# Optimization experiments

Hardware: AMD Instinct MI355X
Metric: run time of the kernel (lower is better)

Reference implementation:

```python
import jax, jax.numpy as jnp
import numpy as np

ALPHA = 4.0  # spikingjelly surrogate.Sigmoid default alpha

@jax.custom_vjp
def heaviside_sg(x):
    # forward: Heaviside (spike); backward: sigmoid surrogate gradient
    return (x >= 0.0).astype(x.dtype)

def _h_fwd(x):
    return heaviside_sg(x), x

def _h_bwd(x, g):
    s = jax.nn.sigmoid(ALPHA * x)
    return (g * ALPHA * s * (1.0 - s),)

heaviside_sg.defvjp(_h_fwd, _h_bwd)

def lif_wta_step(v, x, tau, vth):
    # charge (decay_input=False, v_reset=0): v = v + x - v/tau
    v = v + x - v / tau
    # winner-take-all fire: only the per-sample argmax neuron may spike
    mask = jax.nn.one_hot(jnp.argmax(v, axis=1), v.shape[1], dtype=v.dtype)
    spike = heaviside_sg(v * mask - vth)
    pre_v = v  # membrane before reset (stored as pre_v)
    # overridden neuronal_reset: reset spike computed WITHOUT WTA mask; hard reset to 0
    reset_spike = heaviside_sg(v - vth)
    v_next = v * (1.0 - reset_spike)
    return v_next, spike, pre_v

def setup_inputs() -> dict:
    key = jax.random.key(0)
    k1, k2, k3 = jax.random.split(key, 3)
    B, C, T = 256, 32, 4000
    x = jax.random.normal(k1, (B, C, T), dtype=jnp.float32)
    # init: normal(mean=0.8, std=0.05) then clamp to [0,1]
    W1 = jnp.clip(0.8 + 0.05 * jax.random.normal(k2, (64, 32), dtype=jnp.float32), 0.0, 1.0)
    W2 = jnp.clip(0.8 + 0.05 * jax.random.normal(k3, (128, 64), dtype=jnp.float32), 0.0, 1.0)
    return {"x": x, "W1": W1, "W2": W2}

def reference(x, W1, W2):
    B = x.shape[0]
    dt = x.dtype
    xt = jnp.transpose(x, (2, 0, 1))  # [T, B, 32]
    carry0 = (jnp.zeros((B, 32), dt), jnp.zeros((B, 64), dt),
              jnp.zeros((B, 128), dt), jnp.zeros((B, 128), dt))

    def step(carry, inp):
        v0, v1, v2, _ = carry
        v0n, s0, _ = lif_wta_step(v0, inp, 3.0, 1.5)      # trans_neuron
        h1 = s0 @ W1.T                                    # [B,64]
        v1n, s1, _ = lif_wta_step(v1, h1, 80000.0, 1.2)   # b1_neuron
        h2 = s1 @ W2.T                                    # [B,128]
        v2n, _, pv2 = lif_wta_step(v2, h2, 80000.0, 1.2)  # b2_neuron
        return (v0n, v1n, v2n, pv2), None

    (_, _, _, pre_v2), _ = jax.lax.scan(step, carry0, xt)
    return jnp.exp(pre_v2)  # liquid_state: exp of last-step pre-reset membrane of b2
```

## Files before the change

### kernel.cpp

```cpp
#include <hip/hip_runtime.h>
#include <cstdint>
#include <cstddef>


#pragma clang fp contract(off)

typedef float f32x4 __attribute__((ext_vector_type(4)));

constexpr int T_TOTAL = 4000;
constexpr int NCH = 32;
constexpr int N1 = 64;
constexpr int N2 = 128;
constexpr int CT = 96;
constexpr int TS0 = 108;
constexpr int TS1 = 100;
constexpr int NCHUNK = (T_TOTAL + CT - 1) / CT;

__device__ __forceinline__ int read_lane_i(int v, int l) {
  return __builtin_amdgcn_readlane(v, l);
}

__global__ __launch_bounds__(512, 1) void lsm_kernel(
    const float* __restrict__ x, const float* __restrict__ W1,
    const float* __restrict__ W2, float* __restrict__ out) {
  __shared__ float w1s[N1 * 33];
  __shared__ float w2s[N2 * 65];
  __shared__ float xs[2][NCH * TS0];
  __shared__ float nv0r[2][NCH * TS1];
  __shared__ float nv1r[2][N1 * TS1];
  __shared__ unsigned j0r[2][CT];
  __shared__ float mpr[2][2][CT];
  __shared__ int   jpr[2][2][CT];

  const int tid = threadIdx.x;
  const int wid = tid >> 6;
  const int lane = tid & 63;
  const int b = blockIdx.x;

  for (int e = tid; e < N1 * NCH; e += 512) w1s[(e >> 5) * 33 + (e & 31)] = W1[e];
  for (int e = tid; e < N2 * N1; e += 512) w2s[(e >> 6) * 65 + (e & 63)] = W2[e];
  if (tid < N1) w1s[tid * 33 + 32] = 0.f;
  if (tid < N2) w2s[tid * 65 + 64] = 0.f;
  __syncthreads();

  const float* xb = x + (size_t)b * (NCH * T_TOTAL);
  constexpr float R3 = 1.0f / 3.0f;
  constexpr float R80 = 1.0f / 80000.0f;

  float nv0p = 0.f;
  float nv1p = 0.f;
  float nv2p = 0.f;

  for (int p = 0; p < NCHUNK + 5; ++p) {
    if (wid == 0) {
      const int c = p - 1;
      if (c >= 0 && c < NCHUNK) {
        const int S = min(CT, T_TOTAL - c * CT);
        const int xl = lane & 31;
        const int hi4 = (lane >> 5) << 2;
        const float* xrow = xs[c & 1] + xl * TS0;
        float* nrow = nv0r[c & 1] + xl * TS1 + hi4;
        f32x4 C0 = *(const f32x4*)(xrow + 0);
        f32x4 C1 = *(const f32x4*)(xrow + 4);
        for (int tb = 0; tb < S; tb += 8) {
          f32x4 N0 = *(const f32x4*)(xrow + tb + 8);
          f32x4 Nx = *(const f32x4*)(xrow + tb + 12);
          float nva[8];
#pragma unroll
          for (int k = 0; k < 8; ++k) {
            float xc = (k < 4) ? C0[k] : C1[k - 4];
            float a  = nv0p + xc;
            float q0 = nv0p * R3;
            float e  = __builtin_fmaf(-3.0f, q0, nv0p);
            float q  = __builtin_fmaf(e, R3, q0);
            bool  r  = nv0p >= 1.5f;
            float f  = a - q;
            nv0p = r ? xc : f;
            nva[k] = nv0p;
          }
          f32x4 wv;
          wv.x = hi4 ? nva[4] : nva[0];
          wv.y = hi4 ? nva[5] : nva[1];
          wv.z = hi4 ? nva[6] : nva[2];
          wv.w = hi4 ? nva[7] : nva[3];
          *(f32x4*)(nrow + tb) = wv;
          C0 = N0; C1 = Nx;
        }
      }
    } else if (wid == 1) {
      const int c = p - 2;
      if (c >= 0 && c < NCHUNK) {
        const int cb = c & 1;
        const float* nvs = nv0r[cb] + lane;
        float m = nvs[0];
        int j = 0;
#pragma unroll 8
        for (int n = 1; n < 32; ++n) {
          float v = nvs[n * TS1];
          bool g = v > m;
          j = g ? n : j;
          m = g ? v : m;
        }
        j0r[cb][lane] = (m >= 1.5f) ? (unsigned)j : 32u;
        if (lane < 32) {
          const float* nvs2 = nv0r[cb] + 64 + lane;
          float m2 = nvs2[0];
          int j2 = 0;
#pragma unroll 8
          for (int n = 1; n < 32; ++n) {
            float v = nvs2[n * TS1];
            bool g = v > m2;
            j2 = g ? n : j2;
            m2 = g ? v : m2;
          }
          j0r[cb][64 + lane] = (m2 >= 1.5f) ? (unsigned)j2 : 32u;
        }
      }
    } else if (wid == 2) {
      const int c = p - 3;
      if (c >= 0 && c < NCHUNK) {
        const int S = min(CT, T_TOTAL - c * CT);
        const int cb = c & 1;
        const int jv  = (int)j0r[cb][lane];
        const int jv2 = (int)j0r[cb][64 + (lane & 31)];
        const float* wrow = w1s + lane * 33;
        float* nrow = nv1r[cb] + lane * TS1;
        float hr[8];
#pragma unroll
        for (int k = 0; k < 8; ++k) hr[k] = wrow[read_lane_i(jv, k)];
        for (int tb = 0; tb < S; tb += 8) {
          const int pb = tb + 8;
          const bool hi = pb >= 64;
          const int src = hi ? jv2 : jv;
          const int pbase = hi ? pb - 64 : pb;
          float nva[8];
#pragma unroll
          for (int k = 0; k < 8; ++k) {
            float h = hr[k];
            hr[k] = wrow[read_lane_i(src, pbase + k)];
            float a = nv1p + h;
            float m = nv1p * R80;
            bool  r = nv1p >= 1.2f;
            float f = a - m;
            nv1p = r ? h : f;
            nva[k] = nv1p;
          }
          f32x4 w0v = {nva[0], nva[1], nva[2], nva[3]};
          f32x4 w1v = {nva[4], nva[5], nva[6], nva[7]};
          *(f32x4*)(nrow + tb) = w0v;
          *(f32x4*)(nrow + tb + 4) = w1v;
        }
      }
    } else if (wid == 3 || wid == 6) {
      const int c = p - 4;
      if (c >= 0 && c < NCHUNK) {
        const int cb = c & 1;
        const int half = (wid == 6) ? 1 : 0;
        const float* nvs = nv1r[cb] + half * 32 * TS1 + lane;
        float m = nvs[0];
        int j = 0;
#pragma unroll 8
        for (int n = 1; n < 32; ++n) {
          float v = nvs[n * TS1];
          bool g = v > m;
          j = g ? n : j;
          m = g ? v : m;
        }
        mpr[cb][half][lane] = m;
        jpr[cb][half][lane] = j;
        if (lane < 32) {
          const float* nvs2 = nv1r[cb] + half * 32 * TS1 + 64 + lane;
          float m2 = nvs2[0];
          int j2 = 0;
#pragma unroll 8
          for (int n = 1; n < 32; ++n) {
            float v = nvs2[n * TS1];
            bool g = v > m2;
            j2 = g ? n : j2;
            m2 = g ? v : m2;
          }
          mpr[cb][half][64 + lane] = m2;
          jpr[cb][half][64 + lane] = j2;
        }
      }
    } else if (wid == 4) {
      const int c = p;
      if (c < NCHUNK) {
        float* dst = xs[c & 1];
        const int g8 = lane >> 3;
        const int tl8 = (lane & 7) << 2;
        f32x4 vr[12];
        bool okv[12];
#pragma unroll
        for (int j = 0; j < 12; ++j) {
          const int k = (j & 3) * 8 + g8;
          const int ts = j >> 2;
          const int tg = c * CT + ts * 32 + tl8;
          const bool ok = (tg + 3) < T_TOTAL;
          okv[j] = ok;
          const int tgs = ok ? tg : 0;
          vr[j] = *reinterpret_cast<const f32x4*>(&xb[(size_t)k * T_TOTAL + tgs]);
        }
#pragma unroll
        for (int j = 0; j < 12; ++j) {
          if (okv[j]) {
            const int k = (j & 3) * 8 + g8;
            const int ts = j >> 2;
            *(f32x4*)(&dst[k * TS0 + ts * 32 + tl8]) = vr[j];
          }
        }
      }
    } else {
      const int c = p - 5;
      if (c >= 0 && c < NCHUNK) {
        const int S = min(CT, T_TOTAL - c * CT);
        const int cb = c & 1;
        float mlo = mpr[cb][0][lane], mhi = mpr[cb][1][lane];
        int jlo = jpr[cb][0][lane], jhi = jpr[cb][1][lane];
        bool g = mhi > mlo;
        float mm = g ? mhi : mlo;
        int jj = g ? (jhi + 32) : jlo;
        const int pkv = (mm >= 1.2f) ? jj : 64;
        const int l32 = 64 + (lane & 31);
        float mlo2 = mpr[cb][0][l32], mhi2 = mpr[cb][1][l32];
        int jlo2 = jpr[cb][0][l32], jhi2 = jpr[cb][1][l32];
        bool g2 = mhi2 > mlo2;
        float mm2 = g2 ? mhi2 : mlo2;
        int jj2 = g2 ? (jhi2 + 32) : jlo2;
        const int pkv2 = (mm2 >= 1.2f) ? jj2 : 64;
        const float* wrow = w2s + (lane + ((wid == 7) ? 64 : 0)) * 65;
        float hr[8];
#pragma unroll
        for (int k = 0; k < 8; ++k) hr[k] = wrow[read_lane_i(pkv, k)];
        for (int tb = 0; tb < S; tb += 8) {
          const int pb = tb + 8;
          const bool hi = pb >= 64;
          const int src = hi ? pkv2 : pkv;
          const int pbase = hi ? pb - 64 : pb;
#pragma unroll
          for (int k = 0; k < 8; ++k) {
            float h = hr[k];
            hr[k] = wrow[read_lane_i(src, pbase + k)];
            float a = nv2p + h;
            float m = nv2p * R80;
            bool  r = nv2p >= 1.2f;
            float f = a - m;
            nv2p = r ? h : f;
          }
        }
      }
    }
    __syncthreads();
  }

  if (wid == 5) out[(size_t)b * N2 + lane] = expf(nv2p);
  if (wid == 7) out[(size_t)b * N2 + 64 + lane] = expf(nv2p);
}

extern "C" void kernel_launch(void* const* d_in, const int* in_sizes, int n_in,
                              void* d_out, int out_size, void* d_ws, size_t ws_size,
                              hipStream_t stream) {
  (void)n_in; (void)out_size; (void)d_ws; (void)ws_size;
  const float* x = (const float*)d_in[0];
  const float* W1 = (const float*)d_in[1];
  const float* W2 = (const float*)d_in[2];
  float* out = (float*)d_out;
  const int B = in_sizes[0] / (NCH * T_TOTAL);
  lsm_kernel<<<dim3(B), dim3(512), 0, stream>>>(x, W1, W2, out);
}
```

Before: 277.7 us.

## Shorten wavefront pipeline: direct global x loads, fused argmax stages, L2 prefetch

Removes the shared-memory x staging stage: warp 0 now reads x directly from global memory with a two-deep register prefetch. The layer-0 argmax is fused into the layer-1 warp, and each argmax warp now handles all 128 timesteps. These changes cut the pipeline from NCHUNK+5 to NCHUNK+3 barrier phases. Chunk size grows from 96 to 128 timesteps to amortize barriers, and warps 1 and 4 become touch-loaders that warm the cache for the next chunk. The risk is global-load latency on warp 0's serial recurrence and longer per-phase critical paths.

```diff
diff --git a/kernel.cpp b/kernel.cpp
--- a/kernel.cpp
+++ b/kernel.cpp
@@ -11,9 +11,8 @@
 constexpr int NCH = 32;
 constexpr int N1 = 64;
 constexpr int N2 = 128;
-constexpr int CT = 96;
-constexpr int TS0 = 108;
-constexpr int TS1 = 100;
+constexpr int CT = 128;
+constexpr int TS1 = 140;
 constexpr int NCHUNK = (T_TOTAL + CT - 1) / CT;
 
 __device__ __forceinline__ int read_lane_i(int v, int l) {
@@ -25,10 +24,8 @@
     const float* __restrict__ W2, float* __restrict__ out) {
   __shared__ float w1s[N1 * 33];
   __shared__ float w2s[N2 * 65];
-  __shared__ float xs[2][NCH * TS0];
   __shared__ float nv0r[2][NCH * TS1];
   __shared__ float nv1r[2][N1 * TS1];
-  __shared__ unsigned j0r[2][CT];
   __shared__ float mpr[2][2][CT];
   __shared__ int   jpr[2][2][CT];
 
@@ -50,21 +47,26 @@
   float nv0p = 0.f;
   float nv1p = 0.f;
   float nv2p = 0.f;
-
-  for (int p = 0; p < NCHUNK + 5; ++p) {
+  float warm = 0.f;
+
+  for (int p = 0; p < NCHUNK + 3; ++p) {
     if (wid == 0) {
-      const int c = p - 1;
-      if (c >= 0 && c < NCHUNK) {
+      const int c = p;
+      if (c < NCHUNK) {
         const int S = min(CT, T_TOTAL - c * CT);
         const int xl = lane & 31;
         const int hi4 = (lane >> 5) << 2;
-        const float* xrow = xs[c & 1] + xl * TS0;
+        const float* xg = xb + (size_t)xl * T_TOTAL + c * CT;
         float* nrow = nv0r[c & 1] + xl * TS1 + hi4;
-        f32x4 C0 = *(const f32x4*)(xrow + 0);
-        f32x4 C1 = *(const f32x4*)(xrow + 4);
+        const int tmax = T_TOTAL - c * CT - 8;
+        f32x4 C0 = *(const f32x4*)(xg + 0);
+        f32x4 C1 = *(const f32x4*)(xg + 4);
+        f32x4 D0 = *(const f32x4*)(xg + 8);
+        f32x4 D1 = *(const f32x4*)(xg + 12);
         for (int tb = 0; tb < S; tb += 8) {
-          f32x4 N0 = *(const f32x4*)(xrow + tb + 8);
-          f32x4 Nx = *(const f32x4*)(xrow + tb + 12);
+          int tp = tb + 16; tp = (tp < tmax) ? tp : tmax;
+          f32x4 E0 = *(const f32x4*)(xg + tp);
+          f32x4 E1 = *(const f32x4*)(xg + tp + 4);
           float nva[8];
 #pragma unroll
           for (int k = 0; k < 8; ++k) {
@@ -84,12 +86,13 @@
           wv.z = hi4 ? nva[6] : nva[2];
           wv.w = hi4 ? nva[7] : nva[3];
           *(f32x4*)(nrow + tb) = wv;
-          C0 = N0; C1 = Nx;
-        }
-      }
-    } else if (wid == 1) {
-      const int c = p - 2;
+          C0 = D0; C1 = D1; D0 = E0; D1 = E1;
+        }
+      }
+    } else if (wid == 2) {
+      const int c = p - 1;
       if (c >= 0 && c < NCHUNK) {
+        const int S = min(CT, T_TOTAL - c * CT);
         const int cb = c & 1;
         const float* nvs = nv0r[cb] + lane;
         float m = nvs[0];
@@ -101,28 +104,18 @@
           j = g ? n : j;
           m = g ? v : m;
         }
-        j0r[cb][lane] = (m >= 1.5f) ? (unsigned)j : 32u;
-        if (lane < 32) {
-          const float* nvs2 = nv0r[cb] + 64 + lane;
-          float m2 = nvs2[0];
-          int j2 = 0;
-#pragma unroll 8
-          for (int n = 1; n < 32; ++n) {
-            float v = nvs2[n * TS1];
-            bool g = v > m2;
-            j2 = g ? n : j2;
-            m2 = g ? v : m2;
-          }
-          j0r[cb][64 + lane] = (m2 >= 1.5f) ? (unsigned)j2 : 32u;
-        }
-      }
-    } else if (wid == 2) {
-      const int c = p - 3;
-      if (c >= 0 && c < NCHUNK) {
-        const int S = min(CT, T_TOTAL - c * CT);
-        const int cb = c & 1;
-        const int jv  = (int)j0r[cb][lane];
-        const int jv2 = (int)j0r[cb][64 + (lane & 31)];
+        const int jv = (m >= 1.5f) ? j : 32;
+        const float* nvs2 = nv0r[cb] + 64 + lane;
+        float m2 = nvs2[0];
+        int j2 = 0;
+#pragma unroll 8
+        for (int n = 1; n < 32; ++n) {
+          float v = nvs2[n * TS1];
+          bool g = v > m2;
+          j2 = g ? n : j2;
+          m2 = g ? v : m2;
+        }
+        const int jv2 = (m2 >= 1.5f) ? j2 : 32;
         const float* wrow = w1s + lane * 33;
         float* nrow = nv1r[cb] + lane * TS1;
         float hr[8];
@@ -139,9 +132,9 @@
             float h = hr[k];
             hr[k] = wrow[read_lane_i(src, pbase + k)];
             float a = nv1p + h;
-            float m = nv1p * R80;
+            float mm = nv1p * R80;
             bool  r = nv1p >= 1.2f;
-            float f = a - m;
+            float f = a - mm;
             nv1p = r ? h : f;
             nva[k] = nv1p;
           }
@@ -152,7 +145,7 @@
         }
       }
     } else if (wid == 3 || wid == 6) {
-      const int c = p - 4;
+      const int c = p - 2;
       if (c >= 0 && c < NCHUNK) {
         const int cb = c & 1;
         const int half = (wid == 6) ? 1 : 0;
@@ -168,50 +161,30 @@
         }
         mpr[cb][half][lane] = m;
         jpr[cb][half][lane] = j;
-        if (lane < 32) {
-          const float* nvs2 = nv1r[cb] + half * 32 * TS1 + 64 + lane;
-          float m2 = nvs2[0];
-          int j2 = 0;
-#pragma unroll 8
-          for (int n = 1; n < 32; ++n) {
-            float v = nvs2[n * TS1];
-            bool g = v > m2;
-            j2 = g ? n : j2;
-            m2 = g ? v : m2;
-          }
-          mpr[cb][half][64 + lane] = m2;
-          jpr[cb][half][64 + lane] = j2;
-        }
-      }
-    } else if (wid == 4) {
-      const int c = p;
-      if (c < NCHUNK) {
-        float* dst = xs[c & 1];
-        const int g8 = lane >> 3;
-        const int tl8 = (lane & 7) << 2;
-        f32x4 vr[12];
-        bool okv[12];
-#pragma unroll
-        for (int j = 0; j < 12; ++j) {
-          const int k = (j & 3) * 8 + g8;
-          const int ts = j >> 2;
-          const int tg = c * CT + ts * 32 + tl8;
-          const bool ok = (tg + 3) < T_TOTAL;
-          okv[j] = ok;
-          const int tgs = ok ? tg : 0;
-          vr[j] = *reinterpret_cast<const f32x4*>(&xb[(size_t)k * T_TOTAL + tgs]);
-        }
-#pragma unroll
-        for (int j = 0; j < 12; ++j) {
-          if (okv[j]) {
-            const int k = (j & 3) * 8 + g8;
-            const int ts = j >> 2;
-            *(f32x4*)(&dst[k * TS0 + ts * 32 + tl8]) = vr[j];
-          }
-        }
+        const float* nvs2 = nvs + 64;
+        float m2 = nvs2[0];
+        int j2 = 0;
+#pragma unroll 8
+        for (int n = 1; n < 32; ++n) {
+          float v = nvs2[n * TS1];
+          bool g = v > m2;
+          j2 = g ? n : j2;
+          m2 = g ? v : m2;
+        }
+        mpr[cb][half][64 + lane] = m2;
+        jpr[cb][half][64 + lane] = j2;
+      }
+    } else if (wid == 1 || wid == 4) {
+      const int c2 = p + 1;
+      if (c2 < NCHUNK) {
+        const int L = lane + ((wid == 4) ? 64 : 0);
+        const int ch = L >> 2;
+        int t = c2 * CT + (L & 3) * 32;
+        t = (t < T_TOTAL) ? t : (T_TOTAL - 1);
+        warm += xb[(size_t)ch * T_TOTAL + t];
       }
     } else {
-      const int c = p - 5;
+      const int c = p - 3;
       if (c >= 0 && c < NCHUNK) {
         const int S = min(CT, T_TOTAL - c * CT);
         const int cb = c & 1;
@@ -221,9 +194,8 @@
         float mm = g ? mhi : mlo;
         int jj = g ? (jhi + 32) : jlo;
         const int pkv = (mm >= 1.2f) ? jj : 64;
-        const int l32 = 64 + (lane & 31);
-        float mlo2 = mpr[cb][0][l32], mhi2 = mpr[cb][1][l32];
-        int jlo2 = jpr[cb][0][l32], jhi2 = jpr[cb][1][l32];
+        float mlo2 = mpr[cb][0][64 + lane], mhi2 = mpr[cb][1][64 + lane];
+        int jlo2 = jpr[cb][0][64 + lane], jhi2 = jpr[cb][1][64 + lane];
         bool g2 = mhi2 > mlo2;
         float mm2 = g2 ? mhi2 : mlo2;
         int jj2 = g2 ? (jhi2 + 32) : jlo2;
@@ -242,9 +214,9 @@
             float h = hr[k];
             hr[k] = wrow[read_lane_i(src, pbase + k)];
             float a = nv2p + h;
-            float m = nv2p * R80;
+            float mv = nv2p * R80;
             bool  r = nv2p >= 1.2f;
-            float f = a - m;
+            float f = a - mv;
             nv2p = r ? h : f;
           }
         }
@@ -255,6 +227,7 @@
 
   if (wid == 5) out[(size_t)b * N2 + lane] = expf(nv2p);
   if (wid == 7) out[(size_t)b * N2 + 64 + lane] = expf(nv2p);
+  asm volatile("" :: "v"(warm));
 }
 
 extern "C" void kernel_launch(void* const* d_in, const int* in_sizes, int n_in,
```

New measurement: 326.0 us. 1.17x slower.

## Replace block-wide barriers with per-stage LDS flag producer/consumer synchronization

Applied to the files above, without the earlier changes.

Replaces the lockstep pipeline, where every chunk ends with __syncthreads across all eight waves, with point-to-point producer/consumer flags in volatile shared memory. Each wave now spins (with s_sleep) only on the stages it depends on and on its double-buffer consumers, so stages no longer wait on the slowest wave every chunk. The layer-0 argmax is also folded into the layer-1 wave, which removes the j0r buffer and the separate wave-1 stage. This adds spin-wait and LDS polling overhead, and it relies on correct memory ordering through the waitcnt and volatile flags.

```diff
diff --git a/kernel.cpp b/kernel.cpp
--- a/kernel.cpp
+++ b/kernel.cpp
@@ -16,6 +16,9 @@
 constexpr int TS1 = 100;
 constexpr int NCHUNK = (T_TOTAL + CT - 1) / CT;
 
+constexpr int P1 = 0, C1 = 1, P2 = 2, C2 = 3, P4 = 4, C4A = 5, C4B = 6,
+              P5 = 7, C5A = 8, C5B = 9, P6 = 10, C6A = 11, C6B = 12;
+
 __device__ __forceinline__ int read_lane_i(int v, int l) {
   return __builtin_amdgcn_readlane(v, l);
 }
@@ -28,9 +31,9 @@
   __shared__ float xs[2][NCH * TS0];
   __shared__ float nv0r[2][NCH * TS1];
   __shared__ float nv1r[2][N1 * TS1];
-  __shared__ unsigned j0r[2][CT];
   __shared__ float mpr[2][2][CT];
   __shared__ int   jpr[2][2][CT];
+  volatile __shared__ int fl[16];
 
   const int tid = threadIdx.x;
   const int wid = tid >> 6;
@@ -41,220 +44,243 @@
   for (int e = tid; e < N2 * N1; e += 512) w2s[(e >> 6) * 65 + (e & 63)] = W2[e];
   if (tid < N1) w1s[tid * 33 + 32] = 0.f;
   if (tid < N2) w2s[tid * 65 + 64] = 0.f;
+  if (tid < 16) fl[tid] = 0;
   __syncthreads();
+
+  auto wait_ge = [&](int idx, int tgt) {
+    if (tgt <= 0) return;
+    while (fl[idx] < tgt) __builtin_amdgcn_s_sleep(1);
+    asm volatile("" ::: "memory");
+    __builtin_amdgcn_sched_barrier(0);
+  };
+  auto publish = [&](int idx, int val) {
+    __builtin_amdgcn_sched_barrier(0);
+    asm volatile("s_waitcnt lgkmcnt(0)" ::: "memory");
+    if (lane == 0) fl[idx] = val;
+  };
 
   const float* xb = x + (size_t)b * (NCH * T_TOTAL);
   constexpr float R3 = 1.0f / 3.0f;
   constexpr float R80 = 1.0f / 80000.0f;
 
-  float nv0p = 0.f;
-  float nv1p = 0.f;
-  float nv2p = 0.f;
-
-  for (int p = 0; p < NCHUNK + 5; ++p) {
-    if (wid == 0) {
-      const int c = p - 1;
-      if (c >= 0 && c < NCHUNK) {
-        const int S = min(CT, T_TOTAL - c * CT);
-        const int xl = lane & 31;
-        const int hi4 = (lane >> 5) << 2;
-        const float* xrow = xs[c & 1] + xl * TS0;
-        float* nrow = nv0r[c & 1] + xl * TS1 + hi4;
-        f32x4 C0 = *(const f32x4*)(xrow + 0);
-        f32x4 C1 = *(const f32x4*)(xrow + 4);
-        for (int tb = 0; tb < S; tb += 8) {
-          f32x4 N0 = *(const f32x4*)(xrow + tb + 8);
-          f32x4 Nx = *(const f32x4*)(xrow + tb + 12);
-          float nva[8];
-#pragma unroll
-          for (int k = 0; k < 8; ++k) {
-            float xc = (k < 4) ? C0[k] : C1[k - 4];
-            float a  = nv0p + xc;
-            float q0 = nv0p * R3;
-            float e  = __builtin_fmaf(-3.0f, q0, nv0p);
-            float q  = __builtin_fmaf(e, R3, q0);
-            bool  r  = nv0p >= 1.5f;
-            float f  = a - q;
-            nv0p = r ? xc : f;
-            nva[k] = nv0p;
-          }
-          f32x4 wv;
-          wv.x = hi4 ? nva[4] : nva[0];
-          wv.y = hi4 ? nva[5] : nva[1];
-          wv.z = hi4 ? nva[6] : nva[2];
-          wv.w = hi4 ? nva[7] : nva[3];
-          *(f32x4*)(nrow + tb) = wv;
-          C0 = N0; C1 = Nx;
-        }
-      }
-    } else if (wid == 1) {
-      const int c = p - 2;
-      if (c >= 0 && c < NCHUNK) {
-        const int cb = c & 1;
-        const float* nvs = nv0r[cb] + lane;
-        float m = nvs[0];
-        int j = 0;
-#pragma unroll 8
-        for (int n = 1; n < 32; ++n) {
-          float v = nvs[n * TS1];
-          bool g = v > m;
-          j = g ? n : j;
-          m = g ? v : m;
-        }
-        j0r[cb][lane] = (m >= 1.5f) ? (unsigned)j : 32u;
-        if (lane < 32) {
-          const float* nvs2 = nv0r[cb] + 64 + lane;
-          float m2 = nvs2[0];
-          int j2 = 0;
-#pragma unroll 8
-          for (int n = 1; n < 32; ++n) {
-            float v = nvs2[n * TS1];
-            bool g = v > m2;
-            j2 = g ? n : j2;
-            m2 = g ? v : m2;
-          }
-          j0r[cb][64 + lane] = (m2 >= 1.5f) ? (unsigned)j2 : 32u;
-        }
-      }
-    } else if (wid == 2) {
-      const int c = p - 3;
-      if (c >= 0 && c < NCHUNK) {
-        const int S = min(CT, T_TOTAL - c * CT);
-        const int cb = c & 1;
-        const int jv  = (int)j0r[cb][lane];
-        const int jv2 = (int)j0r[cb][64 + (lane & 31)];
-        const float* wrow = w1s + lane * 33;
-        float* nrow = nv1r[cb] + lane * TS1;
-        float hr[8];
-#pragma unroll
-        for (int k = 0; k < 8; ++k) hr[k] = wrow[read_lane_i(jv, k)];
-        for (int tb = 0; tb < S; tb += 8) {
-          const int pb = tb + 8;
-          const bool hi = pb >= 64;
-          const int src = hi ? jv2 : jv;
-          const int pbase = hi ? pb - 64 : pb;
-          float nva[8];
-#pragma unroll
-          for (int k = 0; k < 8; ++k) {
-            float h = hr[k];
-            hr[k] = wrow[read_lane_i(src, pbase + k)];
-            float a = nv1p + h;
-            float m = nv1p * R80;
-            bool  r = nv1p >= 1.2f;
-            float f = a - m;
-            nv1p = r ? h : f;
-            nva[k] = nv1p;
-          }
-          f32x4 w0v = {nva[0], nva[1], nva[2], nva[3]};
-          f32x4 w1v = {nva[4], nva[5], nva[6], nva[7]};
-          *(f32x4*)(nrow + tb) = w0v;
-          *(f32x4*)(nrow + tb + 4) = w1v;
-        }
-      }
-    } else if (wid == 3 || wid == 6) {
-      const int c = p - 4;
-      if (c >= 0 && c < NCHUNK) {
-        const int cb = c & 1;
-        const int half = (wid == 6) ? 1 : 0;
-        const float* nvs = nv1r[cb] + half * 32 * TS1 + lane;
-        float m = nvs[0];
-        int j = 0;
-#pragma unroll 8
-        for (int n = 1; n < 32; ++n) {
-          float v = nvs[n * TS1];
-          bool g = v > m;
-          j = g ? n : j;
-          m = g ? v : m;
-        }
-        mpr[cb][half][lane] = m;
-        jpr[cb][half][lane] = j;
-        if (lane < 32) {
-          const float* nvs2 = nv1r[cb] + half * 32 * TS1 + 64 + lane;
-          float m2 = nvs2[0];
-          int j2 = 0;
-#pragma unroll 8
-          for (int n = 1; n < 32; ++n) {
-            float v = nvs2[n * TS1];
-            bool g = v > m2;
-            j2 = g ? n : j2;
-            m2 = g ? v : m2;
-          }
-          mpr[cb][half][64 + lane] = m2;
-          jpr[cb][half][64 + lane] = j2;
-        }
-      }
-    } else if (wid == 4) {
-      const int c = p;
-      if (c < NCHUNK) {
-        float* dst = xs[c & 1];
-        const int g8 = lane >> 3;
-        const int tl8 = (lane & 7) << 2;
-        f32x4 vr[12];
-        bool okv[12];
-#pragma unroll
-        for (int j = 0; j < 12; ++j) {
+  if (wid == 4) {
+    const int g8 = lane >> 3;
+    const int tl8 = (lane & 7) << 2;
+    for (int c = 0; c < NCHUNK; ++c) {
+      wait_ge(C1, c - 1);
+      float* dst = xs[c & 1];
+      f32x4 vr[12];
+      bool okv[12];
+#pragma unroll
+      for (int j = 0; j < 12; ++j) {
+        const int k = (j & 3) * 8 + g8;
+        const int ts = j >> 2;
+        const int tg = c * CT + ts * 32 + tl8;
+        const bool ok = (tg + 3) < T_TOTAL;
+        okv[j] = ok;
+        const int tgs = ok ? tg : 0;
+        vr[j] = *reinterpret_cast<const f32x4*>(&xb[(size_t)k * T_TOTAL + tgs]);
+      }
+#pragma unroll
+      for (int j = 0; j < 12; ++j) {
+        if (okv[j]) {
           const int k = (j & 3) * 8 + g8;
           const int ts = j >> 2;
-          const int tg = c * CT + ts * 32 + tl8;
-          const bool ok = (tg + 3) < T_TOTAL;
-          okv[j] = ok;
-          const int tgs = ok ? tg : 0;
-          vr[j] = *reinterpret_cast<const f32x4*>(&xb[(size_t)k * T_TOTAL + tgs]);
-        }
-#pragma unroll
-        for (int j = 0; j < 12; ++j) {
-          if (okv[j]) {
-            const int k = (j & 3) * 8 + g8;
-            const int ts = j >> 2;
-            *(f32x4*)(&dst[k * TS0 + ts * 32 + tl8]) = vr[j];
-          }
-        }
-      }
-    } else {
-      const int c = p - 5;
-      if (c >= 0 && c < NCHUNK) {
-        const int S = min(CT, T_TOTAL - c * CT);
-        const int cb = c & 1;
-        float mlo = mpr[cb][0][lane], mhi = mpr[cb][1][lane];
-        int jlo = jpr[cb][0][lane], jhi = jpr[cb][1][lane];
-        bool g = mhi > mlo;
-        float mm = g ? mhi : mlo;
-        int jj = g ? (jhi + 32) : jlo;
-        const int pkv = (mm >= 1.2f) ? jj : 64;
-        const int l32 = 64 + (lane & 31);
-        float mlo2 = mpr[cb][0][l32], mhi2 = mpr[cb][1][l32];
-        int jlo2 = jpr[cb][0][l32], jhi2 = jpr[cb][1][l32];
-        bool g2 = mhi2 > mlo2;
-        float mm2 = g2 ? mhi2 : mlo2;
-        int jj2 = g2 ? (jhi2 + 32) : jlo2;
-        const int pkv2 = (mm2 >= 1.2f) ? jj2 : 64;
-        const float* wrow = w2s + (lane + ((wid == 7) ? 64 : 0)) * 65;
-        float hr[8];
-#pragma unroll
-        for (int k = 0; k < 8; ++k) hr[k] = wrow[read_lane_i(pkv, k)];
-        for (int tb = 0; tb < S; tb += 8) {
-          const int pb = tb + 8;
-          const bool hi = pb >= 64;
-          const int src = hi ? pkv2 : pkv;
-          const int pbase = hi ? pb - 64 : pb;
-#pragma unroll
-          for (int k = 0; k < 8; ++k) {
-            float h = hr[k];
-            hr[k] = wrow[read_lane_i(src, pbase + k)];
-            float a = nv2p + h;
-            float m = nv2p * R80;
-            bool  r = nv2p >= 1.2f;
-            float f = a - m;
-            nv2p = r ? h : f;
-          }
-        }
-      }
-    }
-    __syncthreads();
+          *(f32x4*)(&dst[k * TS0 + ts * 32 + tl8]) = vr[j];
+        }
+      }
+      publish(P1, c + 1);
+    }
+  } else if (wid == 0) {
+    float nv0p = 0.f;
+    const int xl = lane & 31;
+    const int hi4 = (lane >> 5) << 2;
+    for (int c = 0; c < NCHUNK; ++c) {
+      wait_ge(P1, c + 1);
+      wait_ge(C2, c - 1);
+      const int S = min(CT, T_TOTAL - c * CT);
+      const float* xrow = xs[c & 1] + xl * TS0;
+      float* nrow = nv0r[c & 1] + xl * TS1 + hi4;
+      f32x4 C0 = *(const f32x4*)(xrow + 0);
+      f32x4 Cb = *(const f32x4*)(xrow + 4);
+      for (int tb = 0; tb < S; tb += 8) {
+        f32x4 N0 = *(const f32x4*)(xrow + tb + 8);
+        f32x4 Nx = *(const f32x4*)(xrow + tb + 12);
+        float nva[8];
+#pragma unroll
+        for (int k = 0; k < 8; ++k) {
+          float xc = (k < 4) ? C0[k] : Cb[k - 4];
+          float a  = nv0p + xc;
+          float q0 = nv0p * R3;
+          float e  = __builtin_fmaf(-3.0f, q0, nv0p);
+          float q  = __builtin_fmaf(e, R3, q0);
+          bool  r  = nv0p >= 1.5f;
+          float f  = a - q;
+          nv0p = r ? xc : f;
+          nva[k] = nv0p;
+        }
+        f32x4 wv;
+        wv.x = hi4 ? nva[4] : nva[0];
+        wv.y = hi4 ? nva[5] : nva[1];
+        wv.z = hi4 ? nva[6] : nva[2];
+        wv.w = hi4 ? nva[7] : nva[3];
+        *(f32x4*)(nrow + tb) = wv;
+        C0 = N0; Cb = Nx;
+      }
+      publish(P2, c + 1);
+      publish(C1, c + 1);
+    }
+  } else if (wid == 2) {
+    float nv1p = 0.f;
+    const float* wrow = w1s + lane * 33;
+    for (int c = 0; c < NCHUNK; ++c) {
+      wait_ge(P2, c + 1);
+      const int S = min(CT, T_TOTAL - c * CT);
+      const int cb = c & 1;
+      const float* nvs = nv0r[cb] + lane;
+      float m = nvs[0];
+      int j = 0;
+#pragma unroll 8
+      for (int n = 1; n < 32; ++n) {
+        float v = nvs[n * TS1];
+        bool g = v > m;
+        j = g ? n : j;
+        m = g ? v : m;
+      }
+      const int jv = (m >= 1.5f) ? j : 32;
+      int jv2 = 32;
+      if (lane < 32) {
+        const float* nvs2 = nv0r[cb] + 64 + lane;
+        float m2 = nvs2[0];
+        int j2 = 0;
+#pragma unroll 8
+        for (int n = 1; n < 32; ++n) {
+          float v = nvs2[n * TS1];
+          bool g = v > m2;
+          j2 = g ? n : j2;
+          m2 = g ? v : m2;
+        }
+        jv2 = (m2 >= 1.5f) ? j2 : 32;
+      }
+      publish(C2, c + 1);
+      wait_ge(C4A, c - 1);
+      wait_ge(C4B, c - 1);
+      float* nrow = nv1r[cb] + lane * TS1;
+      float hr[8];
+#pragma unroll
+      for (int k = 0; k < 8; ++k) hr[k] = wrow[read_lane_i(jv, k)];
+      for (int tb = 0; tb < S; tb += 8) {
+        const int pb = tb + 8;
+        const bool hi = pb >= 64;
+        const int src = hi ? jv2 : jv;
+        const int pbase = hi ? pb - 64 : pb;
+        float nva[8];
+#pragma unroll
+        for (int k = 0; k < 8; ++k) {
+          float h = hr[k];
+          hr[k] = wrow[read_lane_i(src, pbase + k)];
+          float a = nv1p + h;
+          float mm = nv1p * R80;
+          bool  r = nv1p >= 1.2f;
+          float f = a - mm;
+          nv1p = r ? h : f;
+          nva[k] = nv1p;
+        }
+        f32x4 w0v = {nva[0], nva[1], nva[2], nva[3]};
+        f32x4 w1v = {nva[4], nva[5], nva[6], nva[7]};
+        *(f32x4*)(nrow + tb) = w0v;
+        *(f32x4*)(nrow + tb + 4) = w1v;
+      }
+      publish(P4, c + 1);
+    }
+  } else if (wid == 3 || wid == 6) {
+    const int half = (wid == 6) ? 1 : 0;
+    const int pMine = (wid == 6) ? P6 : P5;
+    const int cMineA = (wid == 6) ? C6A : C5A;
+    const int cMineB = (wid == 6) ? C6B : C5B;
+    const int cBack = (wid == 6) ? C4B : C4A;
+    for (int c = 0; c < NCHUNK; ++c) {
+      wait_ge(P4, c + 1);
+      wait_ge(cMineA, c - 1);
+      wait_ge(cMineB, c - 1);
+      const int cb = c & 1;
+      const float* nvs = nv1r[cb] + half * 32 * TS1 + lane;
+      float m = nvs[0];
+      int j = 0;
+#pragma unroll 8
+      for (int n = 1; n < 32; ++n) {
+        float v = nvs[n * TS1];
+        bool g = v > m;
+        j = g ? n : j;
+        m = g ? v : m;
+      }
+      mpr[cb][half][lane] = m;
+      jpr[cb][half][lane] = j;
+      if (lane < 32) {
+        const float* nvs2 = nvs + 64;
+        float m2 = nvs2[0];
+        int j2 = 0;
+#pragma unroll 8
+        for (int n = 1; n < 32; ++n) {
+          float v = nvs2[n * TS1];
+          bool g = v > m2;
+          j2 = g ? n : j2;
+          m2 = g ? v : m2;
+        }
+        mpr[cb][half][64 + lane] = m2;
+        jpr[cb][half][64 + lane] = j2;
+      }
+      publish(pMine, c + 1);
+      publish(cBack, c + 1);
+    }
+  } else if (wid == 5 || wid == 7) {
+    float nv2p = 0.f;
+    const float* wrow = w2s + (lane + ((wid == 7) ? 64 : 0)) * 65;
+    const int c5 = (wid == 7) ? C5B : C5A;
+    const int c6 = (wid == 7) ? C6B : C6A;
+    for (int c = 0; c < NCHUNK; ++c) {
+      wait_ge(P5, c + 1);
+      wait_ge(P6, c + 1);
+      const int S = min(CT, T_TOTAL - c * CT);
+      const int cb = c & 1;
+      float mlo = mpr[cb][0][lane], mhi = mpr[cb][1][lane];
+      int jlo = jpr[cb][0][lane], jhi = jpr[cb][1][lane];
+      bool g = mhi > mlo;
+      float mm = g ? mhi : mlo;
+      int jj = g ? (jhi + 32) : jlo;
+      const int pkv = (mm >= 1.2f) ? jj : 64;
+      const int l32 = 64 + (lane & 31);
+      float mlo2 = mpr[cb][0][l32], mhi2 = mpr[cb][1][l32];
+      int jlo2 = jpr[cb][0][l32], jhi2 = jpr[cb][1][l32];
+      bool g2 = mhi2 > mlo2;
+      float mm2 = g2 ? mhi2 : mlo2;
+      int jj2 = g2 ? (jhi2 + 32) : jlo2;
+      const int pkv2 = (mm2 >= 1.2f) ? jj2 : 64;
+      float hr[8];
+#pragma unroll
+      for (int k = 0; k < 8; ++k) hr[k] = wrow[read_lane_i(pkv, k)];
+      for (int tb = 0; tb < S; tb += 8) {
+        const int pb = tb + 8;
+        const bool hi = pb >= 64;
+        const int src = hi ? pkv2 : pkv;
+        const int pbase = hi ? pb - 64 : pb;
+#pragma unroll
+        for (int k = 0; k < 8; ++k) {
+          float h = hr[k];
+          hr[k] = wrow[read_lane_i(src, pbase + k)];
+          float a = nv2p + h;
+          float mv = nv2p * R80;
+          bool  r = nv2p >= 1.2f;
+          float f = a - mv;
+          nv2p = r ? h : f;
+        }
+      }
+      publish(c5, c + 1);
+      publish(c6, c + 1);
+    }
+    const int row = lane + ((wid == 7) ? 64 : 0);
+    out[(size_t)b * N2 + row] = expf(nv2p);
   }
-
-  if (wid == 5) out[(size_t)b * N2 + lane] = expf(nv2p);
-  if (wid == 7) out[(size_t)b * N2 + 64 + lane] = expf(nv2p);
 }
 
 extern "C" void kernel_launch(void* const* d_in, const int* in_sizes, int n_in,
```

After: 339.8 us. 1.22x slower.
